# Performance work log

Hardware: AMD Instinct MI355X
Metric: run time of the kernel (lower is better)

## Reference

```python
import jax, jax.numpy as jnp
import numpy as np

VERY_SMALL_NUMBER = 1e12  # undefined global in source; conventional large mask value
NEG_SLOPE = 0.2           # LeakyReLU(0.2) default act

N, F_IN, F_OUT = 8192, 128, 64


def setup_inputs() -> dict:
    key = jax.random.key(0)
    k1, k2, k3, k4 = jax.random.split(key, 4)
    h = jax.random.normal(k1, (N, F_IN), dtype=jnp.float32)
    adj = jax.random.normal(k2, (N, N), dtype=jnp.float32)  # ~half entries > 0
    # xavier_uniform with gain=1.414, approximated with scaled normals
    w = jax.random.normal(k3, (F_IN, F_OUT), dtype=jnp.float32) * (1.414 * np.sqrt(2.0 / (F_IN + F_OUT)))
    a = jax.random.normal(k4, (2 * F_OUT, 1), dtype=jnp.float32) * (1.414 * np.sqrt(2.0 / (2 * F_OUT + 1)))
    return {"h": h, "adj": adj, "w": w, "a": a}


def reference(h, adj, w, a):
    # GAT v1: e_ij = LeakyReLU(a^T [Wh_i || Wh_j])
    Wh = h @ w                                   # (N, F_OUT)
    a_src, a_dst = a[:F_OUT], a[F_OUT:]          # (F_OUT,1) each
    # a^T[Wh_i||Wh_j] = (Wh a_src)_i + (Wh a_dst)_j  -> broadcast, avoids (N,N,2F) tensor
    e = jax.nn.leaky_relu((Wh @ a_src) + (Wh @ a_dst).T, negative_slope=NEG_SLOPE)  # (N,N)
    attention = jnp.where(adj > 0, e, -VERY_SMALL_NUMBER)
    attention = jax.nn.softmax(attention, axis=1)
    # dropout omitted (eval mode)
    return attention
```

## Files before the change

kernel.cpp:

```cpp
#include <hip/hip_runtime.h>

#define N       8192
#define F_IN    128
#define F_OUT   64
#define NEG_SLOPE 0.2f
#define VERY_SMALL 1.0e12f

__global__ void prep_kernel(const float* __restrict__ w, const float* __restrict__ a,
                            float* __restrict__ ws, float* __restrict__ wd) {
    int k = threadIdx.x;
    float s = 0.f, d = 0.f;
#pragma unroll
    for (int j = 0; j < F_OUT; ++j) {
        float wv = w[k * F_OUT + j];
        s += wv * a[j];
        d += wv * a[F_OUT + j];
    }
    ws[k] = s;
    wd[k] = d;
}

__global__ void srcdst_kernel(const float* __restrict__ h, const float* __restrict__ ws,
                              const float* __restrict__ wd,
                              float* __restrict__ src, float* __restrict__ dst) {
    __shared__ float sws[F_IN], swd[F_IN];
    int t = threadIdx.x;
    if (t < F_IN) { sws[t] = ws[t]; swd[t] = wd[t]; }
    __syncthreads();
    int i = blockIdx.x * blockDim.x + t;
    const float4* h4 = reinterpret_cast<const float4*>(h + (size_t)i * F_IN);
    float s = 0.f, d = 0.f;
#pragma unroll
    for (int k4 = 0; k4 < F_IN / 4; ++k4) {
        float4 hv = h4[k4];
        s += hv.x * sws[k4*4+0] + hv.y * sws[k4*4+1] + hv.z * sws[k4*4+2] + hv.w * sws[k4*4+3];
        d += hv.x * swd[k4*4+0] + hv.y * swd[k4*4+1] + hv.z * swd[k4*4+2] + hv.w * swd[k4*4+3];
    }
    src[i] = s;
    dst[i] = d;
}

__device__ __forceinline__ float waveReduceMax(float x) {
#pragma unroll
    for (int off = 32; off > 0; off >>= 1) x = fmaxf(x, __shfl_xor(x, off));
    return x;
}
__device__ __forceinline__ float waveReduceSum(float x) {
#pragma unroll
    for (int off = 32; off > 0; off >>= 1) x += __shfl_xor(x, off);
    return x;
}

__global__ __launch_bounds__(256) void row_softmax_kernel(
        const float* __restrict__ adj, const float* __restrict__ src,
        const float* __restrict__ dst, float* __restrict__ out) {
    const int row = blockIdx.x;
    const int t   = threadIdx.x;
    const size_t base = (size_t)row * N;

    const float si = src[row];

    const float4* adj4 = reinterpret_cast<const float4*>(adj + base);
    const float4* dst4 = reinterpret_cast<const float4*>(dst);

    float v[32];
    float lmax = -VERY_SMALL;

#pragma unroll
    for (int it = 0; it < 8; ++it) {
        const int idx4 = it * 256 + t;
        float4 av = adj4[idx4];
        float4 dv = dst4[idx4];

        float e0 = si + dv.x; e0 = (e0 > 0.f) ? e0 : NEG_SLOPE * e0;
        float e1 = si + dv.y; e1 = (e1 > 0.f) ? e1 : NEG_SLOPE * e1;
        float e2 = si + dv.z; e2 = (e2 > 0.f) ? e2 : NEG_SLOPE * e2;
        float e3 = si + dv.w; e3 = (e3 > 0.f) ? e3 : NEG_SLOPE * e3;

        float m0 = (av.x > 0.f) ? e0 : -VERY_SMALL;
        float m1 = (av.y > 0.f) ? e1 : -VERY_SMALL;
        float m2 = (av.z > 0.f) ? e2 : -VERY_SMALL;
        float m3 = (av.w > 0.f) ? e3 : -VERY_SMALL;

        v[it*4+0] = m0; v[it*4+1] = m1; v[it*4+2] = m2; v[it*4+3] = m3;
        lmax = fmaxf(lmax, fmaxf(fmaxf(m0, m1), fmaxf(m2, m3)));
    }

    __shared__ float sred[4];
    float wm = waveReduceMax(lmax);
    const int wave = t >> 6;
    if ((t & 63) == 0) sred[wave] = wm;
    __syncthreads();
    const float rmax = fmaxf(fmaxf(sred[0], sred[1]), fmaxf(sred[2], sred[3]));
    __syncthreads();

    float lsum = 0.f;
#pragma unroll
    for (int k = 0; k < 32; ++k) {
        v[k] = __expf(v[k] - rmax);
        lsum += v[k];
    }

    float wsum = waveReduceSum(lsum);
    if ((t & 63) == 0) sred[wave] = wsum;
    __syncthreads();
    const float rsum = sred[0] + sred[1] + sred[2] + sred[3];
    const float inv = 1.0f / rsum;

    float4* out4 = reinterpret_cast<float4*>(out + base);
#pragma unroll
    for (int it = 0; it < 8; ++it) {
        const int idx4 = it * 256 + t;
        float4 o;
        o.x = v[it*4+0] * inv;
        o.y = v[it*4+1] * inv;
        o.z = v[it*4+2] * inv;
        o.w = v[it*4+3] * inv;
        out4[idx4] = o;
    }
}

extern "C" void kernel_launch(void* const* d_in, const int* in_sizes, int n_in,
                              void* d_out, int out_size, void* d_ws, size_t ws_size,
                              hipStream_t stream) {
    const float* h   = (const float*)d_in[0];
    const float* adj = (const float*)d_in[1];
    const float* w   = (const float*)d_in[2];
    const float* a   = (const float*)d_in[3];
    float* out = (float*)d_out;

    float* W   = (float*)d_ws;
    float* wsv = W;
    float* wdv = W + F_IN;
    float* src = W + 2 * F_IN;
    float* dst = W + 2 * F_IN + N;

    prep_kernel<<<1, F_IN, 0, stream>>>(w, a, wsv, wdv);
    srcdst_kernel<<<N / 256, 256, 0, stream>>>(h, wsv, wdv, src, dst);
    row_softmax_kernel<<<N, 256, 0, stream>>>(adj, src, dst, out);
}
```

Before: 446.6 us.

## Fuse prep into srcdst, process two rows per block, use nontemporal loads/stores

Folds the tiny weight-projection prep kernel into the srcdst kernel, so each block recomputes w·a itself and one launch is removed. The row softmax kernel now handles two rows per 512-thread block, so each dst vector load is shared by both rows. The adj reads and output writes use nontemporal hints to avoid polluting the cache with streaming data. The cost is redundant w·a work in every srcdst block and a larger block with more synchronisation participants.

```diff
diff --git a/kernel.cpp b/kernel.cpp
--- a/kernel.cpp
+++ b/kernel.cpp
@@ -6,33 +6,31 @@
 #define NEG_SLOPE 0.2f
 #define VERY_SMALL 1.0e12f
 
-__global__ void prep_kernel(const float* __restrict__ w, const float* __restrict__ a,
-                            float* __restrict__ ws, float* __restrict__ wd) {
-    int k = threadIdx.x;
-    float s = 0.f, d = 0.f;
+typedef float fv4 __attribute__((ext_vector_type(4)));
+
+__global__ __launch_bounds__(128) void srcdst_kernel(
+        const float* __restrict__ h, const float* __restrict__ w,
+        const float* __restrict__ a,
+        float* __restrict__ src, float* __restrict__ dst) {
+    __shared__ float sws[F_IN], swd[F_IN];
+    const int t = threadIdx.x;
+    {
+        float s = 0.f, d = 0.f;
 #pragma unroll
-    for (int j = 0; j < F_OUT; ++j) {
-        float wv = w[k * F_OUT + j];
-        s += wv * a[j];
-        d += wv * a[F_OUT + j];
+        for (int j = 0; j < F_OUT; ++j) {
+            float wv = w[t * F_OUT + j];
+            s += wv * a[j];
+            d += wv * a[F_OUT + j];
+        }
+        sws[t] = s; swd[t] = d;
     }
-    ws[k] = s;
-    wd[k] = d;
-}
-
-__global__ void srcdst_kernel(const float* __restrict__ h, const float* __restrict__ ws,
-                              const float* __restrict__ wd,
-                              float* __restrict__ src, float* __restrict__ dst) {
-    __shared__ float sws[F_IN], swd[F_IN];
-    int t = threadIdx.x;
-    if (t < F_IN) { sws[t] = ws[t]; swd[t] = wd[t]; }
     __syncthreads();
-    int i = blockIdx.x * blockDim.x + t;
-    const float4* h4 = reinterpret_cast<const float4*>(h + (size_t)i * F_IN);
+    const int i = blockIdx.x * 128 + t;
+    const fv4* h4 = reinterpret_cast<const fv4*>(h + (size_t)i * F_IN);
     float s = 0.f, d = 0.f;
 #pragma unroll
     for (int k4 = 0; k4 < F_IN / 4; ++k4) {
-        float4 hv = h4[k4];
+        fv4 hv = h4[k4];
         s += hv.x * sws[k4*4+0] + hv.y * sws[k4*4+1] + hv.z * sws[k4*4+2] + hv.w * sws[k4*4+3];
         d += hv.x * swd[k4*4+0] + hv.y * swd[k4*4+1] + hv.z * swd[k4*4+2] + hv.w * swd[k4*4+3];
     }
@@ -51,72 +49,86 @@
     return x;
 }
 
-__global__ __launch_bounds__(256) void row_softmax_kernel(
+__global__ __launch_bounds__(512) void row_softmax_kernel(
         const float* __restrict__ adj, const float* __restrict__ src,
         const float* __restrict__ dst, float* __restrict__ out) {
-    const int row = blockIdx.x;
-    const int t   = threadIdx.x;
-    const size_t base = (size_t)row * N;
+    const int r0 = blockIdx.x * 2;
+    const int t  = threadIdx.x;
+    const float s0 = src[r0];
+    const float s1 = src[r0 + 1];
 
-    const float si = src[row];
+    const fv4* adjA = reinterpret_cast<const fv4*>(adj + (size_t)r0 * N);
+    const fv4* adjB = reinterpret_cast<const fv4*>(adj + (size_t)(r0 + 1) * N);
+    const fv4* dst4 = reinterpret_cast<const fv4*>(dst);
 
-    const float4* adj4 = reinterpret_cast<const float4*>(adj + base);
-    const float4* dst4 = reinterpret_cast<const float4*>(dst);
-
-    float v[32];
-    float lmax = -VERY_SMALL;
+    float v0[16], v1[16];
+    float lm0 = -VERY_SMALL, lm1 = -VERY_SMALL;
 
 #pragma unroll
-    for (int it = 0; it < 8; ++it) {
-        const int idx4 = it * 256 + t;
-        float4 av = adj4[idx4];
-        float4 dv = dst4[idx4];
+    for (int it = 0; it < 4; ++it) {
+        const int idx4 = it * 512 + t;
+        fv4 dv = dst4[idx4];
+        fv4 aA = __builtin_nontemporal_load(&adjA[idx4]);
+        fv4 aB = __builtin_nontemporal_load(&adjB[idx4]);
 
-        float e0 = si + dv.x; e0 = (e0 > 0.f) ? e0 : NEG_SLOPE * e0;
-        float e1 = si + dv.y; e1 = (e1 > 0.f) ? e1 : NEG_SLOPE * e1;
-        float e2 = si + dv.z; e2 = (e2 > 0.f) ? e2 : NEG_SLOPE * e2;
-        float e3 = si + dv.w; e3 = (e3 > 0.f) ? e3 : NEG_SLOPE * e3;
+        float e;
+        e = s0 + dv.x; e = (e > 0.f) ? e : NEG_SLOPE * e; float a0 = (aA.x > 0.f) ? e : -VERY_SMALL;
+        e = s0 + dv.y; e = (e > 0.f) ? e : NEG_SLOPE * e; float a1 = (aA.y > 0.f) ? e : -VERY_SMALL;
+        e = s0 + dv.z; e = (e > 0.f) ? e : NEG_SLOPE * e; float a2 = (aA.z > 0.f) ? e : -VERY_SMALL;
+        e = s0 + dv.w; e = (e > 0.f) ? e : NEG_SLOPE * e; float a3 = (aA.w > 0.f) ? e : -VERY_SMALL;
+        e = s1 + dv.x; e = (e > 0.f) ? e : NEG_SLOPE * e; float b0 = (aB.x > 0.f) ? e : -VERY_SMALL;
+        e = s1 + dv.y; e = (e > 0.f) ? e : NEG_SLOPE * e; float b1 = (aB.y > 0.f) ? e : -VERY_SMALL;
+        e = s1 + dv.z; e = (e > 0.f) ? e : NEG_SLOPE * e; float b2 = (aB.z > 0.f) ? e : -VERY_SMALL;
+        e = s1 + dv.w; e = (e > 0.f) ? e : NEG_SLOPE * e; float b3 = (aB.w > 0.f) ? e : -VERY_SMALL;
 
-        float m0 = (av.x > 0.f) ? e0 : -VERY_SMALL;
-        float m1 = (av.y > 0.f) ? e1 : -VERY_SMALL;
-        float m2 = (av.z > 0.f) ? e2 : -VERY_SMALL;
-        float m3 = (av.w > 0.f) ? e3 : -VERY_SMALL;
-
-        v[it*4+0] = m0; v[it*4+1] = m1; v[it*4+2] = m2; v[it*4+3] = m3;
-        lmax = fmaxf(lmax, fmaxf(fmaxf(m0, m1), fmaxf(m2, m3)));
+        v0[it*4+0] = a0; v0[it*4+1] = a1; v0[it*4+2] = a2; v0[it*4+3] = a3;
+        v1[it*4+0] = b0; v1[it*4+1] = b1; v1[it*4+2] = b2; v1[it*4+3] = b3;
+        lm0 = fmaxf(lm0, fmaxf(fmaxf(a0, a1), fmaxf(a2, a3)));
+        lm1 = fmaxf(lm1, fmaxf(fmaxf(b0, b1), fmaxf(b2, b3)));
     }
 
-    __shared__ float sred[4];
-    float wm = waveReduceMax(lmax);
+    __shared__ float smax[2][8], ssum[2][8];
     const int wave = t >> 6;
-    if ((t & 63) == 0) sred[wave] = wm;
+    float wm0 = waveReduceMax(lm0);
+    float wm1 = waveReduceMax(lm1);
+    if ((t & 63) == 0) { smax[0][wave] = wm0; smax[1][wave] = wm1; }
     __syncthreads();
-    const float rmax = fmaxf(fmaxf(sred[0], sred[1]), fmaxf(sred[2], sred[3]));
-    __syncthreads();
-
-    float lsum = 0.f;
+    float rmax0 = smax[0][0], rmax1 = smax[1][0];
 #pragma unroll
-    for (int k = 0; k < 32; ++k) {
-        v[k] = __expf(v[k] - rmax);
-        lsum += v[k];
+    for (int k = 1; k < 8; ++k) {
+        rmax0 = fmaxf(rmax0, smax[0][k]);
+        rmax1 = fmaxf(rmax1, smax[1][k]);
     }
 
-    float wsum = waveReduceSum(lsum);
-    if ((t & 63) == 0) sred[wave] = wsum;
+    float ls0 = 0.f, ls1 = 0.f;
+#pragma unroll
+    for (int k = 0; k < 16; ++k) {
+        v0[k] = __expf(v0[k] - rmax0); ls0 += v0[k];
+        v1[k] = __expf(v1[k] - rmax1); ls1 += v1[k];
+    }
+
+    float ws0 = waveReduceSum(ls0);
+    float ws1 = waveReduceSum(ls1);
+    if ((t & 63) == 0) { ssum[0][wave] = ws0; ssum[1][wave] = ws1; }
     __syncthreads();
-    const float rsum = sred[0] + sred[1] + sred[2] + sred[3];
-    const float inv = 1.0f / rsum;
+    float rs0 = ssum[0][0], rs1 = ssum[1][0];
+#pragma unroll
+    for (int k = 1; k < 8; ++k) { rs0 += ssum[0][k]; rs1 += ssum[1][k]; }
+    const float inv0 = 1.0f / rs0;
+    const float inv1 = 1.0f / rs1;
 
-    float4* out4 = reinterpret_cast<float4*>(out + base);
+    fv4* outA = reinterpret_cast<fv4*>(out + (size_t)r0 * N);
+    fv4* outB = reinterpret_cast<fv4*>(out + (size_t)(r0 + 1) * N);
 #pragma unroll
-    for (int it = 0; it < 8; ++it) {
-        const int idx4 = it * 256 + t;
-        float4 o;
-        o.x = v[it*4+0] * inv;
-        o.y = v[it*4+1] * inv;
-        o.z = v[it*4+2] * inv;
-        o.w = v[it*4+3] * inv;
-        out4[idx4] = o;
+    for (int it = 0; it < 4; ++it) {
+        const int idx4 = it * 512 + t;
+        fv4 oA, oB;
+        oA.x = v0[it*4+0] * inv0; oA.y = v0[it*4+1] * inv0;
+        oA.z = v0[it*4+2] * inv0; oA.w = v0[it*4+3] * inv0;
+        oB.x = v1[it*4+0] * inv1; oB.y = v1[it*4+1] * inv1;
+        oB.z = v1[it*4+2] * inv1; oB.w = v1[it*4+3] * inv1;
+        __builtin_nontemporal_store(oA, &outA[idx4]);
+        __builtin_nontemporal_store(oB, &outB[idx4]);
     }
 }
 
@@ -130,12 +142,9 @@
     float* out = (float*)d_out;
 
     float* W   = (float*)d_ws;
-    float* wsv = W;
-    float* wdv = W + F_IN;
-    float* src = W + 2 * F_IN;
-    float* dst = W + 2 * F_IN + N;
+    float* src = W;
+    float* dst = W + N;
 
-    prep_kernel<<<1, F_IN, 0, stream>>>(w, a, wsv, wdv);
-    srcdst_kernel<<<N / 256, 256, 0, stream>>>(h, wsv, wdv, src, dst);
-    row_softmax_kernel<<<N, 256, 0, stream>>>(adj, src, dst, out);
+    srcdst_kernel<<<N / 128, 128, 0, stream>>>(h, w, a, src, dst);
+    row_softmax_kernel<<<N / 2, 512, 0, stream>>>(adj, src, dst, out);
 }
```

After: 429.6 us. 3.8% less time.
